# Performance work log

Hardware: AMD Instinct MI355X
Metric: run time of the kernel (lower is better)

Reference implementation:

```python
import jax
import jax.numpy as jnp
import numpy as np
from jax import lax

# Butterworth order-2 lowpass, Wn=0.25 (scipy.signal.butter(2, 0.25))
_B = [0.0976310729378175, 0.195262145875635, 0.0976310729378175]
_A = [1.0, -0.9428090415820634, 0.33333333333333337]


def setup_inputs() -> dict:
    key = jax.random.key(0)
    x = jax.random.normal(key, (128, 8, 32768), dtype=jnp.float32)
    b = jnp.array(_B, dtype=jnp.float32)
    a = jnp.array(_A, dtype=jnp.float32)
    return {"x": x, "b": b, "a": a}


def _odd_ext(x, n):
    # scipy-style odd extension along the last axis
    left = 2.0 * x[..., :1] - x[..., 1:n + 1][..., ::-1]
    right = 2.0 * x[..., -1:] - x[..., -n - 1:-1][..., ::-1]
    return jnp.concatenate([left, x, right], axis=-1)


def _lfilter(b, a, x):
    # Direct-form II transposed IIR filter along last axis, zero initial state.
    b = b / a[0]
    a = a / a[0]
    order = b.shape[0] - 1  # static
    b_tail, a_tail = b[1:], a[1:]
    z0 = jnp.zeros(x.shape[:-1] + (order,), dtype=x.dtype)
    xT = jnp.moveaxis(x, -1, 0)  # [T, ...batch]

    def step(z, xt):
        yt = b[0] * xt + z[..., 0]
        z_shift = jnp.concatenate([z[..., 1:], jnp.zeros_like(z[..., :1])], axis=-1)
        z_new = z_shift + b_tail * xt[..., None] - a_tail * yt[..., None]
        return z_new, yt

    _, yT = lax.scan(step, z0, xT)
    return jnp.moveaxis(yT, 0, -1)


def _filtfilt(x, a, b):
    y = _lfilter(b, a, x)
    y = _lfilter(b, a, y[..., ::-1])
    return y[..., ::-1]


def reference(x, b, a):
    scale = jnp.max(jnp.abs(x), axis=-1, keepdims=True)
    xn = x / scale
    padlen = 3 * max(int(a.shape[0]), int(b.shape[0]))  # static = 9
    xe = _odd_ext(xn, padlen)
    y = _filtfilt(xe, a, b)
    y = y[..., padlen:-padlen]
    return y * scale
```

## Files before the change

### kernel.cpp

```cpp
#include <hip/hip_runtime.h>


#define N_COLS 32768
#define PAD 9
#define LTOT  (N_COLS + 2 * PAD)
#define WF 16
#define WB 16
#define C  32
#define LANES 64
#define P   (C * LANES)
#define NSEG (N_COLS / P)
#define WIN (WF + C + WB)
#define NLD (WIN / 4)
#define WPB 4
#define TPB 256

__launch_bounds__(TPB, 4)
__global__ void filtfilt_kernel(const float* __restrict__ x,
                                const float* __restrict__ bco,
                                const float* __restrict__ aco,
                                float* __restrict__ out,
                                int rows) {
    const int tid = threadIdx.x;
    const int wid = tid >> 6;
    const int lane = tid & 63;
    const int W = blockIdx.x * WPB + wid;
    const int row = W >> 4;
    const int seg = W & (NSEG - 1);
    if (row >= rows) return;

    const float inv_a0 = 1.0f / aco[0];
    const float B0 = bco[0] * inv_a0;
    const float B1 = bco[1] * inv_a0;
    const float B2 = bco[2] * inv_a0;
    const float A1 = aco[1] * inv_a0;
    const float A2 = aco[2] * inv_a0;

    const float* __restrict__ xrow = x + (size_t)row * N_COLS;
    const int xbase = seg * P + C * lane - WF;

    float v[WIN];
#pragma unroll
    for (int j = 0; j < NLD; ++j) {
        int idx = xbase + 4 * j;
        idx = (idx < 0) ? 0 : idx;
        idx = (idx > N_COLS - 4) ? (N_COLS - 4) : idx;
        *(float4*)(v + 4 * j) = *(const float4*)(xrow + idx);
    }

    if (seg == 0 && lane == 0) {
        const float x0 = xrow[0];
#pragma unroll
        for (int k = 0; k < WF; ++k) {
            const int t = k - (WF - PAD);
            v[k] = (t < 0) ? 0.0f : (2.0f * x0 - xrow[PAD - t]);
        }
    }
    if (seg == NSEG - 1 && lane == LANES - 1) {
        const float xl = xrow[N_COLS - 1];
#pragma unroll
        for (int k = 48; k < 57; ++k)
            v[k] = 2.0f * xl - xrow[32814 - k];
#pragma unroll
        for (int k = 57; k < WIN; ++k) v[k] = 0.0f;
    }

    {
        float z0 = 0.0f, z1 = 0.0f;
#pragma unroll
        for (int k = 0; k < WIN; ++k) {
            const float xv = v[k];
            const float y = fmaf(B0, xv, z0);
            z0 = fmaf(-A1, y, fmaf(B1, xv, z1));
            z1 = fmaf(B2, xv, -A2 * y);
            if (k >= WF) v[k] = y;
        }
    }

    if (seg == NSEG - 1 && lane == LANES - 1) {
#pragma unroll
        for (int k = 57; k < WIN; ++k) v[k] = 0.0f;
    }

    {
        float z0 = 0.0f, z1 = 0.0f;
#pragma unroll
        for (int k = WIN - 1; k >= WF; --k) {
            const float xv = v[k];
            const float y = fmaf(B0, xv, z0);
            z0 = fmaf(-A1, y, fmaf(B1, xv, z1));
            z1 = fmaf(B2, xv, -A2 * y);
            if (k < WF + C) v[k] = y;
        }
    }

    float* __restrict__ orow = out + (size_t)row * N_COLS + (xbase + WF);
#pragma unroll
    for (int j = 0; j < C / 4; ++j)
        *(float4*)(orow + 4 * j) = *(const float4*)(v + WF + 4 * j);
}

extern "C" void kernel_launch(void* const* d_in, const int* in_sizes, int n_in,
                              void* d_out, int out_size, void* d_ws, size_t ws_size,
                              hipStream_t stream) {
    const float* x = (const float*)d_in[0];
    const float* b = (const float*)d_in[1];
    const float* a = (const float*)d_in[2];
    float* out = (float*)d_out;
    const int rows = out_size / N_COLS;
    const int total_waves = rows * NSEG;
    const int blocks = (total_waves + WPB - 1) / WPB;
    filtfilt_kernel<<<blocks, TPB, 0, stream>>>(x, b, a, out, rows);
}
```

Before: 252.4 us.

## Stage per-wave slices through swizzled LDS for coalesced loads and stores

Each wave now loads its whole contiguous slice (segment plus halos) into LDS with coalesced float4 accesses. Each lane then reads its local window from LDS using an XOR swizzle to reduce bank conflicts. Results are written back through LDS so global stores are coalesced. The per-lane chunk drops from 32 to 16, which doubles the wave count and raises the launch-bounds occupancy target, at the cost of a larger fraction of redundant halo filtering. Wave-level ordering relies only on compiler fences, not workgroup barriers, which is safe only if the hardware keeps LDS accesses within a wave in order.

Result: faster. 231.8 us (-8.2%).

```diff
diff --git a/kernel.cpp b/kernel.cpp
--- a/kernel.cpp
+++ b/kernel.cpp
@@ -6,26 +6,35 @@
 #define LTOT  (N_COLS + 2 * PAD)
 #define WF 16
 #define WB 16
-#define C  32
+#define C  16
 #define LANES 64
 #define P   (C * LANES)
 #define NSEG (N_COLS / P)
 #define WIN (WF + C + WB)
-#define NLD (WIN / 4)
+#define SLICE (WF + P + WB)
+#define NV4 (SLICE / 4)
 #define WPB 4
 #define TPB 256
 
-__launch_bounds__(TPB, 4)
+#define SWZ(s) ((s) ^ ((((s) >> 4) & 7) << 2))
+
+#define LDS_PHASE_FENCE() do { asm volatile("" ::: "memory"); \
+                               __builtin_amdgcn_sched_barrier(0); } while (0)
+
+__launch_bounds__(TPB, 8)
 __global__ void filtfilt_kernel(const float* __restrict__ x,
                                 const float* __restrict__ bco,
                                 const float* __restrict__ aco,
                                 float* __restrict__ out,
                                 int rows) {
+    __shared__ __align__(128) float xs_all[WPB][SLICE];
     const int tid = threadIdx.x;
     const int wid = tid >> 6;
     const int lane = tid & 63;
+    float* __restrict__ xs = xs_all[wid];
+
     const int W = blockIdx.x * WPB + wid;
-    const int row = W >> 4;
+    const int row = W >> 5;
     const int seg = W & (NSEG - 1);
     if (row >= rows) return;
 
@@ -37,34 +46,36 @@
     const float A2 = aco[2] * inv_a0;
 
     const float* __restrict__ xrow = x + (size_t)row * N_COLS;
-    const int xbase = seg * P + C * lane - WF;
+    const int xoff = seg * P - WF;
 
+#pragma unroll
+    for (int m = 0; m < 5; ++m) {
+        int i = lane + LANES * m;
+        i = (i > NV4 - 1) ? (NV4 - 1) : i;
+        int g = xoff + 4 * i;
+        g = (g < 0) ? 0 : g;
+        g = (g > N_COLS - 4) ? (N_COLS - 4) : g;
+        *(float4*)(xs + SWZ(4 * i)) = *(const float4*)(xrow + g);
+    }
+    LDS_PHASE_FENCE();
+
+    if (seg == 0 && lane < WF) {
+        const int t = lane - (WF - PAD);
+        xs[SWZ(lane)] = (t < 0) ? 0.0f : (2.0f * xrow[0] - xrow[PAD - t]);
+    }
+    if (seg == NSEG - 1 && lane < WF) {
+        const int s = SLICE - WF + lane;
+        xs[SWZ(s)] = (lane < PAD)
+                   ? (2.0f * xrow[N_COLS - 1] - xrow[N_COLS - 2 - lane])
+                   : 0.0f;
+    }
+    LDS_PHASE_FENCE();
+
+    const int s0 = C * lane;
     float v[WIN];
 #pragma unroll
-    for (int j = 0; j < NLD; ++j) {
-        int idx = xbase + 4 * j;
-        idx = (idx < 0) ? 0 : idx;
-        idx = (idx > N_COLS - 4) ? (N_COLS - 4) : idx;
-        *(float4*)(v + 4 * j) = *(const float4*)(xrow + idx);
-    }
-
-    if (seg == 0 && lane == 0) {
-        const float x0 = xrow[0];
-#pragma unroll
-        for (int k = 0; k < WF; ++k) {
-            const int t = k - (WF - PAD);
-            v[k] = (t < 0) ? 0.0f : (2.0f * x0 - xrow[PAD - t]);
-        }
-    }
-    if (seg == NSEG - 1 && lane == LANES - 1) {
-        const float xl = xrow[N_COLS - 1];
-#pragma unroll
-        for (int k = 48; k < 57; ++k)
-            v[k] = 2.0f * xl - xrow[32814 - k];
-#pragma unroll
-        for (int k = 57; k < WIN; ++k) v[k] = 0.0f;
-    }
-
+    for (int j = 0; j < WIN / 4; ++j)
+        *(float4*)(v + 4 * j) = *(const float4*)(xs + SWZ(s0 + 4 * j));
     {
         float z0 = 0.0f, z1 = 0.0f;
 #pragma unroll
@@ -76,12 +87,10 @@
             if (k >= WF) v[k] = y;
         }
     }
-
     if (seg == NSEG - 1 && lane == LANES - 1) {
 #pragma unroll
-        for (int k = 57; k < WIN; ++k) v[k] = 0.0f;
+        for (int k = 41; k < WIN; ++k) v[k] = 0.0f;
     }
-
     {
         float z0 = 0.0f, z1 = 0.0f;
 #pragma unroll
@@ -93,11 +102,19 @@
             if (k < WF + C) v[k] = y;
         }
     }
+    LDS_PHASE_FENCE();
 
-    float* __restrict__ orow = out + (size_t)row * N_COLS + (xbase + WF);
 #pragma unroll
     for (int j = 0; j < C / 4; ++j)
-        *(float4*)(orow + 4 * j) = *(const float4*)(v + WF + 4 * j);
+        *(float4*)(xs + SWZ(s0 + WF + 4 * j)) = *(const float4*)(v + WF + 4 * j);
+    LDS_PHASE_FENCE();
+
+    float* __restrict__ orow = out + (size_t)row * N_COLS + seg * P;
+#pragma unroll
+    for (int m = 0; m < P / 4 / LANES; ++m) {
+        const int i = lane + LANES * m;
+        *(float4*)(orow + 4 * i) = *(const float4*)(xs + SWZ(WF + 4 * i));
+    }
 }
 
 extern "C" void kernel_launch(void* const* d_in, const int* in_sizes, int n_in,
@@ -109,6 +126,6 @@
     float* out = (float*)d_out;
     const int rows = out_size / N_COLS;
     const int total_waves = rows * NSEG;
-    const int blocks = (total_waves + WPB - 1) / WPB;
+    const int blocks = total_waves / WPB;
     filtfilt_kernel<<<blocks, TPB, 0, stream>>>(x, b, a, out, rows);
 }
```
